# Performance work log

Measured on AMD Instinct MI355X. Metric: run time of the kernel, lower is better.

## Reference

```python
import jax, jax.numpy as jnp
import numpy as np

N = 131072   # total inner-graph nodes (G * n)
G = 2048     # number of inner graphs = nodes of outer graph fg
n = 64       # nodes per inner graph (contiguous blocks)
E = 1048576  # inner edges
EF = 32768   # outer (fg) edges
D = 128      # emb_dim == hidden_dim
K = 8        # SortPooling k
VOCAB = 150


def setup_inputs() -> dict:
    key = jax.random.key(0)
    ks = jax.random.split(key, 32)
    p = lambda k, shape: (jax.random.normal(k, shape, jnp.float32) * 0.1)
    inp = {
        'h': jax.random.randint(ks[0], (N,), 0, VOCAB),
        'g_src': jax.random.randint(ks[1], (E,), 0, N),
        'g_dst': jax.random.randint(ks[2], (E,), 0, N),
        'fg_src': jax.random.randint(ks[3], (EF,), 0, G),
        'fg_dst': jax.random.randint(ks[4], (EF,), 0, G),
        'token_emb': p(ks[5], (VOCAB, D)),
        # GATConv 1 (D -> D, 1 head): fc weight (in,out), attn vectors, output bias
        'W1': p(ks[6], (D, D)), 'al1': p(ks[7], (D,)), 'ar1': p(ks[8], (D,)), 'b1': p(ks[9], (D,)),
        # GATConv 2
        'W2': p(ks[10], (D, D)), 'al2': p(ks[11], (D,)), 'ar2': p(ks[12], (D,)), 'b2': p(ks[13], (D,)),
        # GATConv 3 (K*D -> D) over fg
        'W3': p(ks[14], (K * D, D)), 'al3': p(ks[15], (D,)), 'ar3': p(ks[16], (D,)), 'b3': p(ks[17], (D,)),
        # linear_forward
        'Wf': p(ks[18], (D, D)), 'bf': p(ks[19], (D,)),
        # linear
        'Wl': p(ks[20], (D, D)), 'bl': p(ks[21], (D,)),
        # linear1
        'Wl1': p(ks[22], (D, D)), 'bl1': p(ks[23], (D,)),
        # clasifier
        'Wc': p(ks[24], (D, 2)), 'bc': p(ks[25], (2,)),
    }
    return inp


def gat_conv(src, dst, num_nodes, x, W, al, ar, b):
    """DGL GATConv, num_heads=1, allow_zero_in_degree=True, no activation."""
    f = x @ W                                   # [N, D] projected features
    el = f @ al                                 # [N] left attention logits
    er = f @ ar                                 # [N] right attention logits
    e = jax.nn.leaky_relu(el[src] + er[dst], 0.2)   # [E] per-edge score
    m = jax.ops.segment_max(e, dst, num_segments=num_nodes)
    a = jnp.exp(e - m[dst])
    s = jax.ops.segment_sum(a, dst, num_segments=num_nodes)
    alpha = a / s[dst]                          # edge softmax over incoming edges
    out = jax.ops.segment_sum(alpha[:, None] * f[src], dst, num_segments=num_nodes)
    return out + b                              # zero-in-degree nodes -> bias only


def sort_pooling(x, num_graphs, nodes_per_graph, k):
    """DGL SortPooling: sort each node's feature ascending, rank nodes by last
    channel descending, take top-k, concat -> [G, k*D]."""
    d = x.shape[-1]
    x = jnp.sort(x.reshape(num_graphs, nodes_per_graph, d), axis=-1)
    idx = jnp.argsort(-x[:, :, -1], axis=1)[:, :k]          # [G, k]
    topk = jnp.take_along_axis(x, idx[:, :, None], axis=1)  # [G, k, D]
    return topk.reshape(num_graphs, k * d)


def reference(h, g_src, g_dst, fg_src, fg_dst, token_emb,
              W1, al1, ar1, b1, W2, al2, ar2, b2, W3, al3, ar3, b3,
              Wf, bf, Wl, bl, Wl1, bl1, Wc, bc):
    x = jax.nn.relu(token_emb[h])                                   # [N, D]
    x = jax.nn.relu(gat_conv(g_src, g_dst, N, x, W1, al1, ar1, b1))
    x = jax.nn.relu(gat_conv(g_src, g_dst, N, x, W2, al2, ar2, b2))
    x = jax.nn.relu(x @ Wf + bf)                                    # linear_forward
    x = sort_pooling(x, G, n, K)                                    # [G, K*D]
    x = jax.nn.relu(gat_conv(fg_src, fg_dst, G, x, W3, al3, ar3, b3))
    x = jax.nn.relu(x @ Wl + bl)                                    # dropout = eval identity
    x = jax.nn.relu(x @ Wl1 + bl1)
    x = x @ Wc + bc
    return x.reshape(-1, 2)
```

## Files before the change

### kernel.cpp

```cpp
#include <hip/hip_runtime.h>
#include <math.h>

#define NN   131072
#define GG   2048
#define NPG  64
#define EE   1048576
#define EFN  32768
#define DD   128
#define KK   8
#define VOCAB 150

typedef unsigned short bfu;
typedef _Float16 f16x8 __attribute__((ext_vector_type(8)));
typedef float f32x4 __attribute__((ext_vector_type(4)));

static __device__ __forceinline__ bfu f2b(float f) {
  unsigned u = __float_as_uint(f);
  u += 0x7FFFu + ((u >> 16) & 1u);
  return (bfu)(u >> 16);
}
static __device__ __forceinline__ float b2f(bfu b) {
  return __uint_as_float(((unsigned)b) << 16);
}

static __device__ __forceinline__ bfu f2h(float f) {
  _Float16 h = (_Float16)f;
  bfu u;
  __builtin_memcpy(&u, &h, 2);
  return u;
}
static __device__ __forceinline__ float h2f(bfu b) {
  _Float16 h;
  __builtin_memcpy(&h, &b, 2);
  return (float)h;
}

__global__ void fill_f32_kernel(float* __restrict__ p, float v, int nElems) {
  int i = blockIdx.x * 256 + threadIdx.x;
  if (i < nElems) p[i] = v;
}

__global__ void zero_int_kernel(int* __restrict__ p, int nElems) {
  int i = blockIdx.x * 256 + threadIdx.x;
  if (i < nElems) p[i] = 0;
}

__global__ void init_softmax_kernel(float* __restrict__ mx, float* __restrict__ sm, int nElems) {
  int i = blockIdx.x * 256 + threadIdx.x;
  if (i < nElems) { mx[i] = -INFINITY; sm[i] = 0.f; }
}

__global__ void embed_relu_kernel(const float* __restrict__ temb,
                                  const int* __restrict__ h,
                                  float* __restrict__ x, int total) {
  int i = blockIdx.x * 256 + threadIdx.x;
  if (i >= total) return;
// ... 88 lines not shown
    float val = red[r][c] + red[r][128 + c];
    out[(size_t)(row0 + r) * 128 + c] = val;
    As[idx] = val * al[c];
    As[4096 + idx] = val * ar[c];
  }
  __syncthreads();
  if (t < 8) {
    float s = 0.f;
    for (int c = 0; c < 128; c++) s += As[t * 128 + c];
    el[row0 + t] = s;
  } else if (t < 16) {
    int r = t - 8;
    float s = 0.f;
    for (int c = 0; c < 128; c++) s += As[4096 + r * 128 + c];
    er[row0 + r] = s;
  }
}

__global__ void pack_w2_kernel(const float* __restrict__ W2, const float* __restrict__ Wf,
                               bfu* __restrict__ w2h, bfu* __restrict__ wfh) {
  int i = blockIdx.x * 256 + threadIdx.x;
  if (i >= 32768) return;
  const float* W = (i < 16384) ? W2 : Wf;
  bfu* dst = (i < 16384) ? w2h : wfh;
  int ii = i & 16383;
  int k = ii >> 7, n = ii & 127;
  bfu h = f2h(W[ii]);
  int kk = k >> 5, k5 = k & 31, quad = k5 >> 3, j = k5 & 7;
  int tt = n >> 4, m16 = n & 15;
  int pos = ((((kk * 8 + tt) * 4 + quad) * 16) + m16) * 8 + j;
  dst[pos] = h;
}

template <int SRC_MODE, int EPI>
__global__ __launch_bounds__(256) void mfma_gemm(
    const float* A, const bfu* __restrict__ WfHi,
    const float* __restrict__ bias, void* out,
    const float* __restrict__ al, const float* __restrict__ ar,
    float* __restrict__ el, float* __restrict__ er,
    float* __restrict__ keyb) {
  const int t = threadIdx.x;
  const int lane = t & 63, wv_ = t >> 6;
  const int m16 = lane & 15, quad = lane >> 4;
  const int rowbase = blockIdx.x * 128 + wv_ * 32;
  const float* arow0 = nullptr;
  const float* arow1 = nullptr;
  const bfu* brow0 = nullptr;
  const bfu* brow1 = nullptr;
  if constexpr (SRC_MODE == 0) {
    arow0 = A + (size_t)(rowbase + m16) * 128;
    arow1 = A + (size_t)(rowbase + 16 + m16) * 128;
  } else {
    brow0 = (const bfu*)A + (size_t)(rowbase + m16) * 128;
    brow1 = (const bfu*)A + (size_t)(rowbase + 16 + m16) * 128;
  }
  f32x4 acc[2][8];
#pragma unroll
  for (int rg = 0; rg < 2; rg++)
#pragma unroll
    for (int i = 0; i < 8; i++) acc[rg][i] = (f32x4){0.f, 0.f, 0.f, 0.f};
#pragma unroll
  for (int kk = 0; kk < 4; kk++) {
    int k0 = kk * 32 + quad * 8;
    f16x8 ahi0, alo0, ahi1, alo1;
    if constexpr (SRC_MODE == 2) {
      ahi0 = *(const f16x8*)(brow0 + k0);
      ahi1 = *(const f16x8*)(brow1 + k0);
    } else {
      float av0[8], av1[8];
      *(float4*)&av0[0] = *(const float4*)(arow0 + k0);
      *(float4*)&av0[4] = *(const float4*)(arow0 + k0 + 4);
      *(float4*)&av1[0] = *(const float4*)(arow1 + k0);
      *(float4*)&av1[4] = *(const float4*)(arow1 + k0 + 4);
#pragma unroll
      for (int i = 0; i < 8; i++) {
        _Float16 h0 = (_Float16)av0[i];
        ahi0[i] = h0;
        alo0[i] = (_Float16)(av0[i] - (float)h0);
        _Float16 h1 = (_Float16)av1[i];
        ahi1[i] = h1;
        alo1[i] = (_Float16)(av1[i] - (float)h1);
      }
    }
#pragma unroll
    for (int tt = 0; tt < 8; tt++) {
      int pos = ((((kk * 8 + tt) * 4 + quad) * 16) + m16) * 8;
      f16x8 bhi = *(const f16x8*)&WfHi[pos];
      acc[0][tt] = __builtin_amdgcn_mfma_f32_16x16x32_f16(ahi0, bhi, acc[0][tt], 0, 0, 0);
      if constexpr (SRC_MODE != 2)
        acc[0][tt] = __builtin_amdgcn_mfma_f32_16x16x32_f16(alo0, bhi, acc[0][tt], 0, 0, 0);
      acc[1][tt] = __builtin_amdgcn_mfma_f32_16x16x32_f16(ahi1, bhi, acc[1][tt], 0, 0, 0);
      if constexpr (SRC_MODE != 2)
        acc[1][tt] = __builtin_amdgcn_mfma_f32_16x16x32_f16(alo1, bhi, acc[1][tt], 0, 0, 0);
    }
  }
#pragma unroll
  for (int rg = 0; rg < 2; rg++) {
    const int rb = rowbase + rg * 16;
    if constexpr (EPI == 1) {
      float pl[4] = {0.f, 0.f, 0.f, 0.f}, pr[4] = {0.f, 0.f, 0.f, 0.f};
#pragma unroll
      for (int tt = 0; tt < 8; tt++) {
        int col = tt * 16 + m16;
        float alv = al[col], arv = ar[col];
#pragma unroll
        for (int r = 0; r < 4; r++) {
          float v = acc[rg][tt][r];
          ((bfu*)out)[(size_t)(rb + quad * 4 + r) * 128 + col] = f2h(v);
          pl[r] += v * alv;
          pr[r] += v * arv;
        }
      }
#pragma unroll
      for (int r = 0; r < 4; r++) {
        float a0 = pl[r], a1 = pr[r];
#pragma unroll
        for (int off = 1; off < 16; off <<= 1) {
          a0 += __shfl_xor(a0, off);
          a1 += __shfl_xor(a1, off);
        }
        if (m16 == 0) {
          el[rb + quad * 4 + r] = a0;
          er[rb + quad * 4 + r] = a1;
        }
      }
    } else {
      float pm[4] = {-INFINITY, -INFINITY, -INFINITY, -INFINITY};
#pragma unroll
      for (int tt = 0; tt < 8; tt++) {
        int col = tt * 16 + m16;
        float bv = bias[col];
#pragma unroll
        for (int r = 0; r < 4; r++) {
          float v = fmaxf(acc[rg][tt][r] + bv, 0.f);
          ((bfu*)out)[(size_t)(rb + quad * 4 + r) * 128 + col] = f2h(v);
          pm[r] = fmaxf(pm[r], v);
        }
      }
#pragma unroll
      for (int r = 0; r < 4; r++) {
        float a0 = pm[r];
#pragma unroll
        for (int off = 1; off < 16; off <<= 1) a0 = fmaxf(a0, __shfl_xor(a0, off));
        if (m16 == 0) keyb[rb + quad * 4 + r] = a0;
      }
    }
  }
}

__global__ __launch_bounds__(64) void attn_logits_kernel(
    const float* __restrict__ f, const float* __restrict__ al,
    const float* __restrict__ ar, float* __restrict__ el,
    float* __restrict__ er) {
  int node = blockIdx.x, lane = threadIdx.x;
  float v1 = f[(size_t)node * 128 + lane];
  float v2 = f[(size_t)node * 128 + 64 + lane];
  float sl = v1 * al[lane] + v2 * al[64 + lane];
  float sr = v1 * ar[lane] + v2 * ar[64 + lane];
#pragma unroll
  for (int off = 32; off; off >>= 1) {
    sl += __shfl_down(sl, off);
    sr += __shfl_down(sr, off);
  }
  if (lane == 0) { el[node] = sl; er[node] = sr; }
}

__global__ void hist_rank_kernel(const int* __restrict__ dst, int* __restrict__ cnt,
                                 int* __restrict__ rank, int nE) {
  int e = blockIdx.x * 256 + threadIdx.x;
  if (e < nE) rank[e] = atomicAdd(&cnt[dst[e]], 1);
}

__global__ __launch_bounds__(256) void scan_block_kernel(
    const int* __restrict__ cnt, int* __restrict__ excl, int* __restrict__ part) {
  __shared__ int s[256];
  int blk = blockIdx.x, tid = threadIdx.x;
  int base = blk * 1024 + tid * 4;
// ... 35 lines not shown
  if (i == 0) row_ptr[n] = total;
}

__global__ __launch_bounds__(256) void scan2048_kernel(const int* __restrict__ cnt,
                                                       int* __restrict__ rp, int total) {
  __shared__ int s[256];
  int t = threadIdx.x;
  int base = t * 8;
  int v[8];
  int tsum = 0;
#pragma unroll
  for (int i = 0; i < 8; i++) { v[i] = cnt[base + i]; tsum += v[i]; }
  s[t] = tsum; __syncthreads();
  for (int off = 1; off < 256; off <<= 1) {
    int x = (t >= off) ? s[t - off] : 0;
    __syncthreads();
    s[t] += x;
    __syncthreads();
  }
  int excl = s[t] - tsum;
#pragma unroll
  for (int i = 0; i < 8; i++) { rp[base + i] = excl; excl += v[i]; }
  if (t == 255) rp[2048] = total;
}

__global__ void scatter2_kernel(const int* __restrict__ dst, const int* __restrict__ src,
                                const int* __restrict__ row_ptr, const int* __restrict__ rank,
                                int* __restrict__ adj_src, int nE) {
  int e = blockIdx.x * 256 + threadIdx.x;
  if (e >= nE) return;
  adj_src[row_ptr[dst[e]] + rank[e]] = src[e];
}

__global__ __launch_bounds__(256) void gat_aggregate_vocab_kernel(
    const bfu* __restrict__ fvh, const float* __restrict__ elv,
    const float* __restrict__ erv, const int* __restrict__ h,
    const int* __restrict__ row_ptr, const int* __restrict__ adj_src,
    const float* __restrict__ bias, bfu* __restrict__ outX) {
  const int t = threadIdx.x;
  const int l = t & 31;
  const int gb = t & 32;
  const int d = blockIdx.x * 8 + (t >> 5);
  const int c0 = l * 4;
  int beg = row_ptr[d];
  int n = row_ptr[d + 1] - beg;
  float4 bv = *(const float4*)&bias[c0];
  if (n == 0) {
    ushort4 o;
    o.x = f2h(fmaxf(bv.x, 0.f)); o.y = f2h(fmaxf(bv.y, 0.f));
    o.z = f2h(fmaxf(bv.z, 0.f)); o.w = f2h(fmaxf(bv.w, 0.f));
    *(ushort4*)&outX[(size_t)d * 128 + c0] = o;
    return;
  }
  float er_d = erv[h[d]];
  float4 acc = make_float4(0.f, 0.f, 0.f, 0.f);
  if (n <= 32) {
    int hv = 0; float sc = -INFINITY;
    if (l < n) {
      hv = h[adj_src[beg + l]];
      float v = elv[hv] + er_d;
      sc = v > 0.f ? v : 0.2f * v;
    }
    float m = sc;
#pragma unroll
    for (int off = 16; off; off >>= 1) m = fmaxf(m, __shfl_xor(m, off));
    float ex = (l < n) ? expf(sc - m) : 0.f;
    float s = ex;
#pragma unroll
    for (int off = 16; off; off >>= 1) s += __shfl_xor(s, off);
    float wt = ex / s;
    for (int j = 0; j < n; j += 4) {
      int   h0 = __shfl(hv, gb + j);
      float w0 = __shfl(wt, gb + j);
      int   j1 = (j + 1 < n) ? j + 1 : j;
      int   h1 = __shfl(hv, gb + j1); float w1 = (j + 1 < n) ? __shfl(wt, gb + j1) : 0.f;
      int   j2 = (j + 2 < n) ? j + 2 : j;
      int   h2 = __shfl(hv, gb + j2); float w2 = (j + 2 < n) ? __shfl(wt, gb + j2) : 0.f;
      int   j3 = (j + 3 < n) ? j + 3 : j;
      int   h3 = __shfl(hv, gb + j3); float w3 = (j + 3 < n) ? __shfl(wt, gb + j3) : 0.f;
      ushort4 f0 = *(const ushort4*)&fvh[(size_t)h0 * 128 + c0];
      ushort4 f1 = *(const ushort4*)&fvh[(size_t)h1 * 128 + c0];
      ushort4 f2 = *(const ushort4*)&fvh[(size_t)h2 * 128 + c0];
      ushort4 f3 = *(const ushort4*)&fvh[(size_t)h3 * 128 + c0];
      acc.x += w0 * h2f(f0.x) + w1 * h2f(f1.x) + w2 * h2f(f2.x) + w3 * h2f(f3.x);
      acc.y += w0 * h2f(f0.y) + w1 * h2f(f1.y) + w2 * h2f(f2.y) + w3 * h2f(f3.y);
      acc.z += w0 * h2f(f0.z) + w1 * h2f(f1.z) + w2 * h2f(f2.z) + w3 * h2f(f3.z);
      acc.w += w0 * h2f(f0.w) + w1 * h2f(f1.w) + w2 * h2f(f2.w) + w3 * h2f(f3.w);
    }
  } else {
    float lm = -INFINITY;
    for (int e = l; e < n; e += 32) {
      int hv = h[adj_src[beg + e]];
      float v = elv[hv] + er_d;
      v = v > 0.f ? v : 0.2f * v;
      lm = fmaxf(lm, v);
    }
#pragma unroll
    for (int off = 16; off; off >>= 1) lm = fmaxf(lm, __shfl_xor(lm, off));
    float ls = 0.f;
    for (int e = l; e < n; e += 32) {
      int hv = h[adj_src[beg + e]];
      float v = elv[hv] + er_d;
      v = v > 0.f ? v : 0.2f * v;
      ls += expf(v - lm);
    }
#pragma unroll
    for (int off = 16; off; off >>= 1) ls += __shfl_xor(ls, off);
    for (int base = 0; base < n; base += 32) {
      int e = base + l;
      int hv = 0; float wt = 0.f;
      if (e < n) {
        hv = h[adj_src[beg + e]];
        float v = elv[hv] + er_d;
        v = v > 0.f ? v : 0.2f * v;
        wt = expf(v - lm) / ls;
      }
      int cnt = min(32, n - base);
      for (int j = 0; j < cnt; ++j) {
        int h0 = __shfl(hv, gb + j);
        float w0 = __shfl(wt, gb + j);
        ushort4 f0 = *(const ushort4*)&fvh[(size_t)h0 * 128 + c0];
        acc.x += w0 * h2f(f0.x);
        acc.y += w0 * h2f(f0.y);
        acc.z += w0 * h2f(f0.z);
        acc.w += w0 * h2f(f0.w);
      }
    }
  }
  ushort4 o;
  o.x = f2h(fmaxf(acc.x + bv.x, 0.f));
  o.y = f2h(fmaxf(acc.y + bv.y, 0.f));
  o.z = f2h(fmaxf(acc.z + bv.z, 0.f));
  o.w = f2h(fmaxf(acc.w + bv.w, 0.f));
  *(ushort4*)&outX[(size_t)d * 128 + c0] = o;
}

__global__ __launch_bounds__(256) void gat_aggregate_csr_kernel(
    const bfu* __restrict__ F, const float* __restrict__ el,
    const float* __restrict__ er, const int* __restrict__ row_ptr,
    const int* __restrict__ adj_src,
    const float* __restrict__ bias, bfu* __restrict__ outX) {
  const int t = threadIdx.x;
  const int l = t & 31;
  const int gb = t & 32;
  const int d = blockIdx.x * 8 + (t >> 5);
  const int c0 = l * 4;
  int beg = row_ptr[d];
  int n = row_ptr[d + 1] - beg;
  float4 bv = *(const float4*)&bias[c0];
  if (n == 0) {
    ushort4 o;
    o.x = f2h(fmaxf(bv.x, 0.f)); o.y = f2h(fmaxf(bv.y, 0.f));
    o.z = f2h(fmaxf(bv.z, 0.f)); o.w = f2h(fmaxf(bv.w, 0.f));
    *(ushort4*)&outX[(size_t)d * 128 + c0] = o;
    return;
  }
  float er_d = er[d];
  float4 acc = make_float4(0.f, 0.f, 0.f, 0.f);
  if (n <= 32) {
    int sv = 0; float sc = -INFINITY;
    if (l < n) {
      sv = adj_src[beg + l];
      float v = el[sv] + er_d;
      sc = v > 0.f ? v : 0.2f * v;
    }
    float m = sc;
#pragma unroll
    for (int off = 16; off; off >>= 1) m = fmaxf(m, __shfl_xor(m, off));
    float ex = (l < n) ? expf(sc - m) : 0.f;
    float s = ex;
#pragma unroll
    for (int off = 16; off; off >>= 1) s += __shfl_xor(s, off);
    float wt = ex / s;
    for (int j = 0; j < n; j += 4) {
      int   s0 = __shfl(sv, gb + j);
      float w0 = __shfl(wt, gb + j);
      int   j1 = (j + 1 < n) ? j + 1 : j;
      int   s1 = __shfl(sv, gb + j1); float w1 = (j + 1 < n) ? __shfl(wt, gb + j1) : 0.f;
      int   j2 = (j + 2 < n) ? j + 2 : j;
      int   s2 = __shfl(sv, gb + j2); float w2 = (j + 2 < n) ? __shfl(wt, gb + j2) : 0.f;
      int   j3 = (j + 3 < n) ? j + 3 : j;
      int   s3 = __shfl(sv, gb + j3); float w3 = (j + 3 < n) ? __shfl(wt, gb + j3) : 0.f;
      ushort4 f0 = *(const ushort4*)&F[(size_t)s0 * 128 + c0];
      ushort4 f1 = *(const ushort4*)&F[(size_t)s1 * 128 + c0];
      ushort4 f2 = *(const ushort4*)&F[(size_t)s2 * 128 + c0];
      ushort4 f3 = *(const ushort4*)&F[(size_t)s3 * 128 + c0];
      acc.x += w0 * h2f(f0.x) + w1 * h2f(f1.x) + w2 * h2f(f2.x) + w3 * h2f(f3.x);
      acc.y += w0 * h2f(f0.y) + w1 * h2f(f1.y) + w2 * h2f(f2.y) + w3 * h2f(f3.y);
      acc.z += w0 * h2f(f0.z) + w1 * h2f(f1.z) + w2 * h2f(f2.z) + w3 * h2f(f3.z);
      acc.w += w0 * h2f(f0.w) + w1 * h2f(f1.w) + w2 * h2f(f2.w) + w3 * h2f(f3.w);
    }
  } else {
    float lm = -INFINITY;
    for (int e = l; e < n; e += 32) {
      int sv = adj_src[beg + e];
      float v = el[sv] + er_d;
      v = v > 0.f ? v : 0.2f * v;
      lm = fmaxf(lm, v);
    }
#pragma unroll
    for (int off = 16; off; off >>= 1) lm = fmaxf(lm, __shfl_xor(lm, off));
    float ls = 0.f;
    for (int e = l; e < n; e += 32) {
      int sv = adj_src[beg + e];
      float v = el[sv] + er_d;
      v = v > 0.f ? v : 0.2f * v;
      ls += expf(v - lm);
    }
#pragma unroll
    for (int off = 16; off; off >>= 1) ls += __shfl_xor(ls, off);
    for (int base = 0; base < n; base += 32) {
      int e = base + l;
      int sv = 0; float wt = 0.f;
      if (e < n) {
        sv = adj_src[beg + e];
        float v = el[sv] + er_d;
        v = v > 0.f ? v : 0.2f * v;
        wt = expf(v - lm) / ls;
      }
      int cnt = min(32, n - base);
      for (int j = 0; j < cnt; ++j) {
        int s0 = __shfl(sv, gb + j);
        float w0 = __shfl(wt, gb + j);
        ushort4 f0 = *(const ushort4*)&F[(size_t)s0 * 128 + c0];
        acc.x += w0 * h2f(f0.x);
        acc.y += w0 * h2f(f0.y);
        acc.z += w0 * h2f(f0.z);
        acc.w += w0 * h2f(f0.w);
      }
    }
  }
  ushort4 o;
  o.x = f2h(fmaxf(acc.x + bv.x, 0.f));
  o.y = f2h(fmaxf(acc.y + bv.y, 0.f));
  o.z = f2h(fmaxf(acc.z + bv.z, 0.f));
  o.w = f2h(fmaxf(acc.w + bv.w, 0.f));
  *(ushort4*)&outX[(size_t)d * 128 + c0] = o;
}

__global__ __launch_bounds__(256) void gat_aggregate_outer_kernel(
    const float* __restrict__ F, const float* __restrict__ el,
    const float* __restrict__ er, const int* __restrict__ row_ptr,
    const int* __restrict__ adj_src,
    const float* __restrict__ bias, float* __restrict__ outG) {
  const int t = threadIdx.x;
  const int l = t & 31;
  const int gb = t & 32;
  const int d = blockIdx.x * 8 + (t >> 5);
  const int c0 = l * 4;
  int beg = row_ptr[d];
  int n = row_ptr[d + 1] - beg;
  float4 bv = *(const float4*)&bias[c0];
  if (n == 0) {
    float4 o;
    o.x = fmaxf(bv.x, 0.f); o.y = fmaxf(bv.y, 0.f);
    o.z = fmaxf(bv.z, 0.f); o.w = fmaxf(bv.w, 0.f);
    *(float4*)&outG[(size_t)d * 128 + c0] = o;
    return;
  }
  float er_d = er[d];
  float4 acc = make_float4(0.f, 0.f, 0.f, 0.f);
  if (n <= 32) {
    int sv = 0; float sc = -INFINITY;
    if (l < n) {
      sv = adj_src[beg + l];
      float v = el[sv] + er_d;
      sc = v > 0.f ? v : 0.2f * v;
    }
    float m = sc;
#pragma unroll
// ... 105 lines not shown
__global__ void bias_relu_kernel(float* __restrict__ x,
                                 const float* __restrict__ b, int total) {
  int i = blockIdx.x * 256 + threadIdx.x;
  if (i >= total) return;
  x[i] = fmaxf(x[i] + b[i & 127], 0.f);
}

__global__ __launch_bounds__(64) void row_max_kernel(const float* __restrict__ x,
                                                     float* __restrict__ key) {
  int node = blockIdx.x, lane = threadIdx.x;
  float v = fmaxf(x[(size_t)node * 128 + lane], x[(size_t)node * 128 + 64 + lane]);
#pragma unroll
  for (int off = 32; off; off >>= 1) v = fmaxf(v, __shfl_down(v, off));
  if (lane == 0) key[node] = v;
}

__global__ __launch_bounds__(64) void select_topk_kernel(
    const float* __restrict__ key, int* __restrict__ sel) {
  __shared__ float keys[NPG];
  int g = blockIdx.x, t = threadIdx.x;
  keys[t] = key[(size_t)g * NPG + t];
  __syncthreads();
  float myk = keys[t];
  int rank = 0;
  for (int j = 0; j < NPG; ++j) {
    float kj = keys[j];
    rank += (kj > myk) || (kj == myk && j < t);
  }
  if (rank < KK) sel[g * KK + rank] = t;
}

__global__ __launch_bounds__(1024) void topk_sort_kernel(
    const float* __restrict__ keyb, const bfu* __restrict__ xin,
    float* __restrict__ xp) {
  __shared__ float keys[NPG];
  __shared__ int sel_l[KK];
  __shared__ float v[1024];
  int g = blockIdx.x, t = threadIdx.x;
  if (t < NPG) keys[t] = keyb[(size_t)g * NPG + t];
  __syncthreads();
  if (t < NPG) {
    float myk = keys[t];
    int rank = 0;
    for (int j = 0; j < NPG; ++j) {
      float kj = keys[j];
      rank += (kj > myk) || (kj == myk && j < t);
    }
    if (rank < KK) sel_l[rank] = t;
  }
  __syncthreads();
  int r = t >> 7, c = t & 127;
  int node = sel_l[r];
  v[t] = h2f(xin[(size_t)(g * NPG + node) * 128 + c]);
  __syncthreads();
  for (int k = 2; k <= 128; k <<= 1) {
    for (int j = k >> 1; j > 0; j >>= 1) {
      int ixj = c ^ j;
      if (ixj > c) {
        float a = v[r * 128 + c], bb = v[r * 128 + ixj];
        bool asc = ((c & k) == 0);
        if (asc ? (a > bb) : (a < bb)) { v[r * 128 + c] = bb; v[r * 128 + ixj] = a; }
      }
      __syncthreads();
    }
  }
  xp[(size_t)g * 1024 + t] = v[t];
}

template <int HF>
__global__ __launch_bounds__(128) void sort_rows_kernel(
    const void* __restrict__ xin, const int* __restrict__ sel,
    float* __restrict__ xp) {
  __shared__ float v[128];
  int b = blockIdx.x;
  int t = threadIdx.x;
  int g = b >> 3, r = b & 7;
  int node = sel[b];
  if (HF) v[t] = h2f(((const bfu*)xin)[(size_t)(g * NPG + node) * 128 + t]);
  else    v[t] = ((const float*)xin)[(size_t)(g * NPG + node) * 128 + t];
  __syncthreads();
  for (int k = 2; k <= 128; k <<= 1) {
    for (int j = k >> 1; j > 0; j >>= 1) {
      int ixj = t ^ j;
      if (ixj > t) {
        float a = v[t], bb = v[ixj];
        bool asc = ((t & k) == 0);
        if (asc ? (a > bb) : (a < bb)) { v[t] = bb; v[ixj] = a; }
      }
      __syncthreads();
    }
  }
  xp[(size_t)g * (KK * 128) + r * 128 + t] = v[t];
}

__global__ __launch_bounds__(128) void mlp_tail_kernel(
    const float* __restrict__ g3, const float* __restrict__ Wl,
    const float* __restrict__ bl, const float* __restrict__ Wl1,
    const float* __restrict__ bl1, const float* __restrict__ Wc,
    const float* __restrict__ bc, float* __restrict__ out) {
// ... 50 lines not shown
  const float* ar2 = (const float*)d_in[12];
  const float* b2 = (const float*)d_in[13];
  const float* W3 = (const float*)d_in[14];
  const float* al3 = (const float*)d_in[15];
  const float* ar3 = (const float*)d_in[16];
  const float* b3 = (const float*)d_in[17];
  const float* Wf = (const float*)d_in[18];
  const float* bfv = (const float*)d_in[19];
  const float* Wl = (const float*)d_in[20];
  const float* bl = (const float*)d_in[21];
  const float* Wl1 = (const float*)d_in[22];
  const float* bl1 = (const float*)d_in[23];
  const float* Wc = (const float*)d_in[24];
  const float* bc = (const float*)d_in[25];
  float* out = (float*)d_out;

  float* ws = (float*)d_ws;
  float* X  = ws;
  float* F  = X + (size_t)NN * DD;
  float* el = F + (size_t)NN * DD;
  float* er = el + NN;
  float* mx = er + NN;
  float* sm = mx + NN;
  int* row_ptr = (int*)(sm + NN);
  int* cursor  = row_ptr + NN + 1;
  int* adj_src = cursor + NN;
  int* part    = adj_src + EE;
  int* rankb = (int*)X;
  bfu* w2h = (bfu*)mx;
  bfu* wfh = w2h + 16384;
  bfu* fvh = wfh + 16384;
  float* elv = (float*)(fvh + VOCAB * 128 + 128);
  float* erv = elv + VOCAB;
  int* ocnt  = (int*)X;
  int* orp   = ocnt + 2048;
  int* orank = orp + 2080;
  int* oadj  = orank + EFN;
  float* xp   = F;
  float* f3   = F + 2097152;
  float* g3   = f3 + (size_t)GG * DD;
  float* t1   = g3 + (size_t)GG * DD;
  float* t2   = t1 + (size_t)GG * DD;
  float* keyb = t2 + (size_t)GG * DD;
  int*   sel  = (int*)(keyb + NN);

  const int totalND = NN * DD;

  if (use_csr) {
    bfu* Fb = (bfu*)F;
    bfu* Xb = (bfu*)X;
    zero_int_kernel<<<NN / 256, 256, 0, stream>>>(cursor, NN);
    hist_rank_kernel<<<EE / 256, 256, 0, stream>>>(g_dst, cursor, rankb, EE);
    scan_block_kernel<<<NN / 1024, 256, 0, stream>>>(cursor, row_ptr, part);
    scan_part_kernel<<<1, 128, 0, stream>>>(part);
    scan_add_kernel<<<(NN + 255) / 256, 256, 0, stream>>>(row_ptr, part, NN, EE);
    scatter2_kernel<<<EE / 256, 256, 0, stream>>>(g_dst, g_src, row_ptr, rankb, adj_src, EE);

    pack_w2_kernel<<<128, 256, 0, stream>>>(W2, Wf, w2h, wfh);
    vocab_l1_kernel<<<VOCAB, 128, 0, stream>>>(temb, W1, al1, ar1, fvh, elv, erv);

    gat_aggregate_vocab_kernel<<<NN / 8, 256, 0, stream>>>(
        fvh, elv, erv, h, row_ptr, adj_src, b1, Xb);

    mfma_gemm<2, 1><<<NN / 128, 256, 0, stream>>>(
        (const float*)X, w2h, nullptr, Fb, al2, ar2, el, er, nullptr);
    gat_aggregate_csr_kernel<<<NN / 8, 256, 0, stream>>>(Fb, el, er, row_ptr, adj_src, b2, Xb);

    mfma_gemm<2, 2><<<NN / 128, 256, 0, stream>>>(
        (const float*)X, wfh, bfv, Xb, nullptr, nullptr, nullptr, nullptr, keyb);

    topk_sort_kernel<<<GG, 1024, 0, stream>>>(keyb, Xb, xp);

    zero_int_kernel<<<GG / 256, 256, 0, stream>>>(ocnt, GG);
    hist_rank_kernel<<<EFN / 256, 256, 0, stream>>>(fg_dst, ocnt, orank, EFN);
    scan2048_kernel<<<1, 256, 0, stream>>>(ocnt, orp, EFN);
    scatter2_kernel<<<EFN / 256, 256, 0, stream>>>(fg_dst, fg_src, orp, orank, oadj, EFN);

    gemm1024_kernel<<<GG / 8, 256, 0, stream>>>(xp, W3, f3, al3, ar3, el, er);
    gat_aggregate_outer_kernel<<<GG / 8, 256, 0, stream>>>(f3, el, er, orp, oadj, b3, g3);

    mlp_tail_kernel<<<GG, 128, 0, stream>>>(g3, Wl, bl, Wl1, bl1, Wc, bc, out);
  } else {
    embed_relu_kernel<<<totalND / 256, 256, 0, stream>>>(temb, h, X, totalND);
    auto gat_inner = [&](const float* W, const float* al, const float* ar, const float* bb) {
      gemm_kernel<DD, 8><<<NN / 8, 128, 0, stream>>>(X, W, nullptr, F, 0);
      attn_logits_kernel<<<NN, 64, 0, stream>>>(F, al, ar, el, er);
      init_softmax_kernel<<<(NN + 255) / 256, 256, 0, stream>>>(mx, sm, NN);
      fill_f32_kernel<<<totalND / 256, 256, 0, stream>>>(X, 0.f, totalND);
      edge_max_kernel<<<(EE + 255) / 256, 256, 0, stream>>>(el, er, g_src, g_dst, mx, EE);
      edge_expsum_kernel<<<(EE + 255) / 256, 256, 0, stream>>>(el, er, mx, g_src, g_dst, sm, EE);
      edge_aggregate_kernel<<<EE, 128, 0, stream>>>(F, el, er, mx, sm, g_src, g_dst, X, EE);
      bias_relu_kernel<<<totalND / 256, 256, 0, stream>>>(X, bb, totalND);
    };
    gat_inner(W1, al1, ar1, b1);
    gat_inner(W2, al2, ar2, b2);
    gemm_kernel<DD, 8><<<NN / 8, 128, 0, stream>>>(X, Wf, bfv, X, 1);
    row_max_kernel<<<NN, 64, 0, stream>>>(X, keyb);

    select_topk_kernel<<<GG, 64, 0, stream>>>(keyb, sel);
    sort_rows_kernel<0><<<GG * KK, 128, 0, stream>>>(X, sel, xp);

    gemm1024_kernel<<<GG / 8, 256, 0, stream>>>(xp, W3, f3, al3, ar3, el, er);
    init_softmax_kernel<<<(GG + 255) / 256, 256, 0, stream>>>(mx, sm, GG);
    fill_f32_kernel<<<(GG * DD + 255) / 256, 256, 0, stream>>>(g3, 0.f, GG * DD);
    edge_max_kernel<<<(EFN + 255) / 256, 256, 0, stream>>>(el, er, fg_src, fg_dst, mx, EFN);
    edge_expsum_kernel<<<(EFN + 255) / 256, 256, 0, stream>>>(el, er, mx, fg_src, fg_dst, sm, EFN);
    edge_aggregate_kernel<<<EFN, 128, 0, stream>>>(f3, el, er, mx, sm, fg_src, fg_dst, g3, EFN);
    bias_relu_kernel<<<(GG * DD + 255) / 256, 256, 0, stream>>>(g3, b3, GG * DD);
    mlp_tail_kernel<<<GG, 128, 0, stream>>>(g3, Wl, bl, Wl1, bl1, Wc, bc, out);
  }
}
// ... 1 lines not shown
```

Before: 425.0 us.

## Fuse GAT aggregation with following MFMA GEMM via LDS tile; MFMA for 1024 GEMM

Merges each inner GAT edge-softmax aggregation with the next projection GEMM. Aggregated rows go into a swizzled 128x128 fp16 LDS tile that feeds MFMA directly, so the intermediate activation no longer round-trips through global memory. The scatter now packs the source node's token id into the high bits of the adjacency entry, which removes the dependent h[] gather in layer 1. The outer 1024-wide GEMM moves to fp16 MFMA using packed W3 and fp16 pooled inputs, trading some precision and adding a 32KB LDS footprint that may lower occupancy.

```diff
diff --git a/kernel.cpp b/kernel.cpp
--- a/kernel.cpp
+++ b/kernel.cpp
@@ -9,19 +9,11 @@
 #define DD   128
 #define KK   8
 #define VOCAB 150
+#define SRCMASK 0x1FFFF
 
 typedef unsigned short bfu;
 typedef _Float16 f16x8 __attribute__((ext_vector_type(8)));
 typedef float f32x4 __attribute__((ext_vector_type(4)));
-
-static __device__ __forceinline__ bfu f2b(float f) {
-  unsigned u = __float_as_uint(f);
-  u += 0x7FFFu + ((u >> 16) & 1u);
-  return (bfu)(u >> 16);
-}
-static __device__ __forceinline__ float b2f(bfu b) {
-  return __uint_as_float(((unsigned)b) << 16);
-}
 
 static __device__ __forceinline__ bfu f2h(float f) {
   _Float16 h = (_Float16)f;
@@ -176,72 +168,162 @@
   dst[pos] = h;
 }
 
-template <int SRC_MODE, int EPI>
-__global__ __launch_bounds__(256) void mfma_gemm(
-    const float* A, const bfu* __restrict__ WfHi,
-    const float* __restrict__ bias, void* out,
+__global__ void pack_wk_kernel(const float* __restrict__ W, bfu* __restrict__ dst, int total) {
+  int i = blockIdx.x * 256 + threadIdx.x;
+  if (i >= total) return;
+  int k = i >> 7, n = i & 127;
+  bfu h = f2h(W[i]);
+  int kk = k >> 5, k5 = k & 31, quad = k5 >> 3, j = k5 & 7;
+  int tt = n >> 4, m16 = n & 15;
+  int pos = ((((kk * 8 + tt) * 4 + quad) * 16) + m16) * 8 + j;
+  dst[pos] = h;
+}
+
+template <int MODE>
+__global__ __launch_bounds__(256) void agg_gemm_kernel(
+    const bfu* __restrict__ Fsrc, const float* __restrict__ elA,
+    const float* __restrict__ erA, const int* __restrict__ h,
+    const int* __restrict__ row_ptr, const int* __restrict__ adj,
+    const float* __restrict__ aggBias, const bfu* __restrict__ Wtab,
     const float* __restrict__ al, const float* __restrict__ ar,
-    float* __restrict__ el, float* __restrict__ er,
+    const float* __restrict__ gemmBias,
+    bfu* __restrict__ outF,
+    float* __restrict__ el_out, float* __restrict__ er_out,
     float* __restrict__ keyb) {
+  __shared__ bfu Atile[128 * 128];
   const int t = threadIdx.x;
+  const int l = t & 31;
+  const int gb = t & 32;
+  const int grp = t >> 5;
+  const int c0 = l * 4;
+  const int blockbase = blockIdx.x * 128;
+  float4 bv = *(const float4*)&aggBias[c0];
+
+  for (int iter = 0; iter < 16; ++iter) {
+    const int dl = iter * 8 + grp;
+    const int d = blockbase + dl;
+    int beg = row_ptr[d];
+    int n = row_ptr[d + 1] - beg;
+    float4 acc = make_float4(0.f, 0.f, 0.f, 0.f);
+    if (n > 0) {
+      float er_d = (MODE == 0) ? erA[h[d]] : erA[d];
+      if (n <= 32) {
+        int idx = 0; float sc = -INFINITY;
+        if (l < n) {
+          int a = adj[beg + l];
+          idx = (MODE == 0) ? (a >> 17) : (a & SRCMASK);
+          float v = elA[idx] + er_d;
+          sc = v > 0.f ? v : 0.2f * v;
+        }
+        float m = sc;
+#pragma unroll
+        for (int off = 16; off; off >>= 1) m = fmaxf(m, __shfl_xor(m, off));
+        float ex = (l < n) ? expf(sc - m) : 0.f;
+        float s = ex;
+#pragma unroll
+        for (int off = 16; off; off >>= 1) s += __shfl_xor(s, off);
+        float wt = ex / s;
+        for (int j = 0; j < n; j += 4) {
+          int   s0 = __shfl(idx, gb + j);
+          float w0 = __shfl(wt, gb + j);
+          int   j1 = (j + 1 < n) ? j + 1 : j;
+          int   s1 = __shfl(idx, gb + j1); float w1 = (j + 1 < n) ? __shfl(wt, gb + j1) : 0.f;
+          int   j2 = (j + 2 < n) ? j + 2 : j;
+          int   s2 = __shfl(idx, gb + j2); float w2 = (j + 2 < n) ? __shfl(wt, gb + j2) : 0.f;
+          int   j3 = (j + 3 < n) ? j + 3 : j;
+          int   s3 = __shfl(idx, gb + j3); float w3 = (j + 3 < n) ? __shfl(wt, gb + j3) : 0.f;
+          ushort4 f0 = *(const ushort4*)&Fsrc[(size_t)s0 * 128 + c0];
+          ushort4 f1 = *(const ushort4*)&Fsrc[(size_t)s1 * 128 + c0];
+          ushort4 f2 = *(const ushort4*)&Fsrc[(size_t)s2 * 128 + c0];
+          ushort4 f3 = *(const ushort4*)&Fsrc[(size_t)s3 * 128 + c0];
+          acc.x += w0 * h2f(f0.x) + w1 * h2f(f1.x) + w2 * h2f(f2.x) + w3 * h2f(f3.x);
+          acc.y += w0 * h2f(f0.y) + w1 * h2f(f1.y) + w2 * h2f(f2.y) + w3 * h2f(f3.y);
+          acc.z += w0 * h2f(f0.z) + w1 * h2f(f1.z) + w2 * h2f(f2.z) + w3 * h2f(f3.z);
+          acc.w += w0 * h2f(f0.w) + w1 * h2f(f1.w) + w2 * h2f(f2.w) + w3 * h2f(f3.w);
+        }
+      } else {
+        float lm = -INFINITY;
+        for (int e = l; e < n; e += 32) {
+          int a = adj[beg + e];
+          int idx = (MODE == 0) ? (a >> 17) : (a & SRCMASK);
+          float v = elA[idx] + er_d;
+          v = v > 0.f ? v : 0.2f * v;
+          lm = fmaxf(lm, v);
+        }
+#pragma unroll
+        for (int off = 16; off; off >>= 1) lm = fmaxf(lm, __shfl_xor(lm, off));
+        float ls = 0.f;
+        for (int e = l; e < n; e += 32) {
+          int a = adj[beg + e];
+          int idx = (MODE == 0) ? (a >> 17) : (a & SRCMASK);
+          float v = elA[idx] + er_d;
+          v = v > 0.f ? v : 0.2f * v;
+          ls += expf(v - lm);
+        }
+#pragma unroll
+        for (int off = 16; off; off >>= 1) ls += __shfl_xor(ls, off);
+        for (int base = 0; base < n; base += 32) {
+          int e = base + l;
+          int idx = 0; float wt = 0.f;
+          if (e < n) {
+            int a = adj[beg + e];
+            idx = (MODE == 0) ? (a >> 17) : (a & SRCMASK);
+            float v = elA[idx] + er_d;
+            v = v > 0.f ? v : 0.2f * v;
+            wt = expf(v - lm) / ls;
+          }
+          int cnt = min(32, n - base);
+          for (int j = 0; j < cnt; ++j) {
+            int s0 = __shfl(idx, gb + j);
+            float w0 = __shfl(wt, gb + j);
+            ushort4 f0 = *(const ushort4*)&Fsrc[(size_t)s0 * 128 + c0];
+            acc.x += w0 * h2f(f0.x);
+            acc.y += w0 * h2f(f0.y);
+            acc.z += w0 * h2f(f0.z);
+            acc.w += w0 * h2f(f0.w);
+          }
+        }
+      }
+    }
+    ushort4 o;
+    o.x = f2h(fmaxf(acc.x + bv.x, 0.f));
+    o.y = f2h(fmaxf(acc.y + bv.y, 0.f));
+    o.z = f2h(fmaxf(acc.z + bv.z, 0.f));
+    o.w = f2h(fmaxf(acc.w + bv.w, 0.f));
+    int chunk = l >> 1;
+    int off = dl * 256 + (((chunk ^ (dl & 15)) << 4)) + ((l & 1) << 3);
+    *(ushort4*)((char*)Atile + off) = o;
+  }
+  __syncthreads();
+
   const int lane = t & 63, wv_ = t >> 6;
   const int m16 = lane & 15, quad = lane >> 4;
-  const int rowbase = blockIdx.x * 128 + wv_ * 32;
-  const float* arow0 = nullptr;
-  const float* arow1 = nullptr;
-  const bfu* brow0 = nullptr;
-  const bfu* brow1 = nullptr;
-  if constexpr (SRC_MODE == 0) {
-    arow0 = A + (size_t)(rowbase + m16) * 128;
-    arow1 = A + (size_t)(rowbase + 16 + m16) * 128;
-  } else {
-    brow0 = (const bfu*)A + (size_t)(rowbase + m16) * 128;
-    brow1 = (const bfu*)A + (size_t)(rowbase + 16 + m16) * 128;
-  }
-  f32x4 acc[2][8];
+  f32x4 acc2[2][8];
 #pragma unroll
   for (int rg = 0; rg < 2; rg++)
 #pragma unroll
-    for (int i = 0; i < 8; i++) acc[rg][i] = (f32x4){0.f, 0.f, 0.f, 0.f};
+    for (int i = 0; i < 8; i++) acc2[rg][i] = (f32x4){0.f, 0.f, 0.f, 0.f};
 #pragma unroll
   for (int kk = 0; kk < 4; kk++) {
-    int k0 = kk * 32 + quad * 8;
-    f16x8 ahi0, alo0, ahi1, alo1;
-    if constexpr (SRC_MODE == 2) {
-      ahi0 = *(const f16x8*)(brow0 + k0);
-      ahi1 = *(const f16x8*)(brow1 + k0);
-    } else {
-      float av0[8], av1[8];
-      *(float4*)&av0[0] = *(const float4*)(arow0 + k0);
-      *(float4*)&av0[4] = *(const float4*)(arow0 + k0 + 4);
-      *(float4*)&av1[0] = *(const float4*)(arow1 + k0);
-      *(float4*)&av1[4] = *(const float4*)(arow1 + k0 + 4);
-#pragma unroll
-      for (int i = 0; i < 8; i++) {
-        _Float16 h0 = (_Float16)av0[i];
-        ahi0[i] = h0;
-        alo0[i] = (_Float16)(av0[i] - (float)h0);
-        _Float16 h1 = (_Float16)av1[i];
-        ahi1[i] = h1;
-        alo1[i] = (_Float16)(av1[i] - (float)h1);
-      }
-    }
+    int cb = kk * 4 + quad;
+    int r0 = wv_ * 32 + m16;
+    int r1 = r0 + 16;
+    int a0 = r0 * 256 + ((cb ^ (r0 & 15)) << 4);
+    int a1 = r1 * 256 + ((cb ^ (r1 & 15)) << 4);
+    f16x8 ahi0 = *(const f16x8*)((char*)Atile + a0);
+    f16x8 ahi1 = *(const f16x8*)((char*)Atile + a1);
 #pragma unroll
     for (int tt = 0; tt < 8; tt++) {
       int pos = ((((kk * 8 + tt) * 4 + quad) * 16) + m16) * 8;
-      f16x8 bhi = *(const f16x8*)&WfHi[pos];
-      acc[0][tt] = __builtin_amdgcn_mfma_f32_16x16x32_f16(ahi0, bhi, acc[0][tt], 0, 0, 0);
-      if constexpr (SRC_MODE != 2)
-        acc[0][tt] = __builtin_amdgcn_mfma_f32_16x16x32_f16(alo0, bhi, acc[0][tt], 0, 0, 0);
-      acc[1][tt] = __builtin_amdgcn_mfma_f32_16x16x32_f16(ahi1, bhi, acc[1][tt], 0, 0, 0);
-      if constexpr (SRC_MODE != 2)
-        acc[1][tt] = __builtin_amdgcn_mfma_f32_16x16x32_f16(alo1, bhi, acc[1][tt], 0, 0, 0);
+      f16x8 bhi = *(const f16x8*)&Wtab[pos];
+      acc2[0][tt] = __builtin_amdgcn_mfma_f32_16x16x32_f16(ahi0, bhi, acc2[0][tt], 0, 0, 0);
+      acc2[1][tt] = __builtin_amdgcn_mfma_f32_16x16x32_f16(ahi1, bhi, acc2[1][tt], 0, 0, 0);
     }
   }
 #pragma unroll
   for (int rg = 0; rg < 2; rg++) {
-    const int rb = rowbase + rg * 16;
-    if constexpr (EPI == 1) {
+    const int rb = blockbase + wv_ * 32 + rg * 16;
+    if constexpr (MODE == 0) {
       float pl[4] = {0.f, 0.f, 0.f, 0.f}, pr[4] = {0.f, 0.f, 0.f, 0.f};
 #pragma unroll
       for (int tt = 0; tt < 8; tt++) {
@@ -249,8 +331,8 @@
         float alv = al[col], arv = ar[col];
 #pragma unroll
         for (int r = 0; r < 4; r++) {
-          float v = acc[rg][tt][r];
-          ((bfu*)out)[(size_t)(rb + quad * 4 + r) * 128 + col] = f2h(v);
+          float v = acc2[rg][tt][r];
+          outF[(size_t)(rb + quad * 4 + r) * 128 + col] = f2h(v);
           pl[r] += v * alv;
           pr[r] += v * arv;
         }
@@ -264,8 +346,8 @@
           a1 += __shfl_xor(a1, off);
         }
         if (m16 == 0) {
-          el[rb + quad * 4 + r] = a0;
-          er[rb + quad * 4 + r] = a1;
+          el_out[rb + quad * 4 + r] = a0;
+          er_out[rb + quad * 4 + r] = a1;
         }
       }
     } else {
@@ -273,11 +355,11 @@
 #pragma unroll
       for (int tt = 0; tt < 8; tt++) {
         int col = tt * 16 + m16;
-        float bv = bias[col];
+        float bvv = gemmBias[col];
 #pragma unroll
         for (int r = 0; r < 4; r++) {
-          float v = fmaxf(acc[rg][tt][r] + bv, 0.f);
-          ((bfu*)out)[(size_t)(rb + quad * 4 + r) * 128 + col] = f2h(v);
+          float v = fmaxf(acc2[rg][tt][r] + bvv, 0.f);
+          outF[(size_t)(rb + quad * 4 + r) * 128 + col] = f2h(v);
           pm[r] = fmaxf(pm[r], v);
         }
       }
@@ -287,6 +369,66 @@
 #pragma unroll
         for (int off = 1; off < 16; off <<= 1) a0 = fmaxf(a0, __shfl_xor(a0, off));
         if (m16 == 0) keyb[rb + quad * 4 + r] = a0;
+      }
+    }
+  }
+}
+
+__global__ __launch_bounds__(256) void mfma_gemm1024_kernel(
+    const bfu* __restrict__ A, const bfu* __restrict__ Wtab,
+    float* __restrict__ out, const float* __restrict__ al,
+    const float* __restrict__ ar, float* __restrict__ el,
+    float* __restrict__ er) {
+  const int t = threadIdx.x;
+  const int lane = t & 63, wv_ = t >> 6;
+  const int m16 = lane & 15, quad = lane >> 4;
+  const int rowbase = blockIdx.x * 128 + wv_ * 32;
+  const bfu* brow0 = A + (size_t)(rowbase + m16) * 1024;
+  const bfu* brow1 = A + (size_t)(rowbase + 16 + m16) * 1024;
+  f32x4 acc[2][8];
+#pragma unroll
+  for (int rg = 0; rg < 2; rg++)
+#pragma unroll
+    for (int i = 0; i < 8; i++) acc[rg][i] = (f32x4){0.f, 0.f, 0.f, 0.f};
+  for (int kk = 0; kk < 32; kk++) {
+    int k0 = kk * 32 + quad * 8;
+    f16x8 ahi0 = *(const f16x8*)(brow0 + k0);
+    f16x8 ahi1 = *(const f16x8*)(brow1 + k0);
+#pragma unroll
+    for (int tt = 0; tt < 8; tt++) {
+      int pos = ((((kk * 8 + tt) * 4 + quad) * 16) + m16) * 8;
+      f16x8 bhi = *(const f16x8*)&Wtab[pos];
+      acc[0][tt] = __builtin_amdgcn_mfma_f32_16x16x32_f16(ahi0, bhi, acc[0][tt], 0, 0, 0);
+      acc[1][tt] = __builtin_amdgcn_mfma_f32_16x16x32_f16(ahi1, bhi, acc[1][tt], 0, 0, 0);
+    }
+  }
+#pragma unroll
+  for (int rg = 0; rg < 2; rg++) {
+    const int rb = rowbase + rg * 16;
+    float pl[4] = {0.f, 0.f, 0.f, 0.f}, pr[4] = {0.f, 0.f, 0.f, 0.f};
+#pragma unroll
+    for (int tt = 0; tt < 8; tt++) {
+      int col = tt * 16 + m16;
+      float alv = al[col], arv = ar[col];
+#pragma unroll
+      for (int r = 0; r < 4; r++) {
+        float v = acc[rg][tt][r];
+        out[(size_t)(rb + quad * 4 + r) * 128 + col] = v;
+        pl[r] += v * alv;
+        pr[r] += v * arv;
+      }
+    }
+#pragma unroll
+    for (int r = 0; r < 4; r++) {
+      float a0 = pl[r], a1 = pr[r];
+#pragma unroll
+      for (int off = 1; off < 16; off <<= 1) {
+        a0 += __shfl_xor(a0, off);
+        a1 += __shfl_xor(a1, off);
+      }
+      if (m16 == 0) {
+        el[rb + quad * 4 + r] = a0;
+        er[rb + quad * 4 + r] = a1;
       }
     }
   }
@@ -388,210 +530,14 @@
   adj_src[row_ptr[dst[e]] + rank[e]] = src[e];
 }
 
-__global__ __launch_bounds__(256) void gat_aggregate_vocab_kernel(
-    const bfu* __restrict__ fvh, const float* __restrict__ elv,
-    const float* __restrict__ erv, const int* __restrict__ h,
-    const int* __restrict__ row_ptr, const int* __restrict__ adj_src,
-    const float* __restrict__ bias, bfu* __restrict__ outX) {
-  const int t = threadIdx.x;
-  const int l = t & 31;
-  const int gb = t & 32;
-  const int d = blockIdx.x * 8 + (t >> 5);
-  const int c0 = l * 4;
-  int beg = row_ptr[d];
-  int n = row_ptr[d + 1] - beg;
-  float4 bv = *(const float4*)&bias[c0];
-  if (n == 0) {
-    ushort4 o;
-    o.x = f2h(fmaxf(bv.x, 0.f)); o.y = f2h(fmaxf(bv.y, 0.f));
-    o.z = f2h(fmaxf(bv.z, 0.f)); o.w = f2h(fmaxf(bv.w, 0.f));
-    *(ushort4*)&outX[(size_t)d * 128 + c0] = o;
-    return;
-  }
-  float er_d = erv[h[d]];
-  float4 acc = make_float4(0.f, 0.f, 0.f, 0.f);
-  if (n <= 32) {
-    int hv = 0; float sc = -INFINITY;
-    if (l < n) {
-      hv = h[adj_src[beg + l]];
-      float v = elv[hv] + er_d;
-      sc = v > 0.f ? v : 0.2f * v;
-    }
-    float m = sc;
-#pragma unroll
-    for (int off = 16; off; off >>= 1) m = fmaxf(m, __shfl_xor(m, off));
-    float ex = (l < n) ? expf(sc - m) : 0.f;
-    float s = ex;
-#pragma unroll
-    for (int off = 16; off; off >>= 1) s += __shfl_xor(s, off);
-    float wt = ex / s;
-    for (int j = 0; j < n; j += 4) {
-      int   h0 = __shfl(hv, gb + j);
-      float w0 = __shfl(wt, gb + j);
-      int   j1 = (j + 1 < n) ? j + 1 : j;
-      int   h1 = __shfl(hv, gb + j1); float w1 = (j + 1 < n) ? __shfl(wt, gb + j1) : 0.f;
-      int   j2 = (j + 2 < n) ? j + 2 : j;
-      int   h2 = __shfl(hv, gb + j2); float w2 = (j + 2 < n) ? __shfl(wt, gb + j2) : 0.f;
-      int   j3 = (j + 3 < n) ? j + 3 : j;
-      int   h3 = __shfl(hv, gb + j3); float w3 = (j + 3 < n) ? __shfl(wt, gb + j3) : 0.f;
-      ushort4 f0 = *(const ushort4*)&fvh[(size_t)h0 * 128 + c0];
-      ushort4 f1 = *(const ushort4*)&fvh[(size_t)h1 * 128 + c0];
-      ushort4 f2 = *(const ushort4*)&fvh[(size_t)h2 * 128 + c0];
-      ushort4 f3 = *(const ushort4*)&fvh[(size_t)h3 * 128 + c0];
-      acc.x += w0 * h2f(f0.x) + w1 * h2f(f1.x) + w2 * h2f(f2.x) + w3 * h2f(f3.x);
-      acc.y += w0 * h2f(f0.y) + w1 * h2f(f1.y) + w2 * h2f(f2.y) + w3 * h2f(f3.y);
-      acc.z += w0 * h2f(f0.z) + w1 * h2f(f1.z) + w2 * h2f(f2.z) + w3 * h2f(f3.z);
-      acc.w += w0 * h2f(f0.w) + w1 * h2f(f1.w) + w2 * h2f(f2.w) + w3 * h2f(f3.w);
-    }
-  } else {
-    float lm = -INFINITY;
-    for (int e = l; e < n; e += 32) {
-      int hv = h[adj_src[beg + e]];
-      float v = elv[hv] + er_d;
-      v = v > 0.f ? v : 0.2f * v;
-      lm = fmaxf(lm, v);
-    }
-#pragma unroll
-    for (int off = 16; off; off >>= 1) lm = fmaxf(lm, __shfl_xor(lm, off));
-    float ls = 0.f;
-    for (int e = l; e < n; e += 32) {
-      int hv = h[adj_src[beg + e]];
-      float v = elv[hv] + er_d;
-      v = v > 0.f ? v : 0.2f * v;
-      ls += expf(v - lm);
-    }
-#pragma unroll
-    for (int off = 16; off; off >>= 1) ls += __shfl_xor(ls, off);
-    for (int base = 0; base < n; base += 32) {
-      int e = base + l;
-      int hv = 0; float wt = 0.f;
-      if (e < n) {
-        hv = h[adj_src[beg + e]];
-        float v = elv[hv] + er_d;
-        v = v > 0.f ? v : 0.2f * v;
-        wt = expf(v - lm) / ls;
-      }
-      int cnt = min(32, n - base);
-      for (int j = 0; j < cnt; ++j) {
-        int h0 = __shfl(hv, gb + j);
-        float w0 = __shfl(wt, gb + j);
-        ushort4 f0 = *(const ushort4*)&fvh[(size_t)h0 * 128 + c0];
-        acc.x += w0 * h2f(f0.x);
-        acc.y += w0 * h2f(f0.y);
-        acc.z += w0 * h2f(f0.z);
-        acc.w += w0 * h2f(f0.w);
-      }
-    }
-  }
-  ushort4 o;
-  o.x = f2h(fmaxf(acc.x + bv.x, 0.f));
-  o.y = f2h(fmaxf(acc.y + bv.y, 0.f));
-  o.z = f2h(fmaxf(acc.z + bv.z, 0.f));
-  o.w = f2h(fmaxf(acc.w + bv.w, 0.f));
-  *(ushort4*)&outX[(size_t)d * 128 + c0] = o;
-}
-
-__global__ __launch_bounds__(256) void gat_aggregate_csr_kernel(
-    const bfu* __restrict__ F, const float* __restrict__ el,
-    const float* __restrict__ er, const int* __restrict__ row_ptr,
-    const int* __restrict__ adj_src,
-    const float* __restrict__ bias, bfu* __restrict__ outX) {
-  const int t = threadIdx.x;
-  const int l = t & 31;
-  const int gb = t & 32;
-  const int d = blockIdx.x * 8 + (t >> 5);
-  const int c0 = l * 4;
-  int beg = row_ptr[d];
-  int n = row_ptr[d + 1] - beg;
-  float4 bv = *(const float4*)&bias[c0];
-  if (n == 0) {
-    ushort4 o;
-    o.x = f2h(fmaxf(bv.x, 0.f)); o.y = f2h(fmaxf(bv.y, 0.f));
-    o.z = f2h(fmaxf(bv.z, 0.f)); o.w = f2h(fmaxf(bv.w, 0.f));
-    *(ushort4*)&outX[(size_t)d * 128 + c0] = o;
-    return;
-  }
-  float er_d = er[d];
-  float4 acc = make_float4(0.f, 0.f, 0.f, 0.f);
-  if (n <= 32) {
-    int sv = 0; float sc = -INFINITY;
-    if (l < n) {
-      sv = adj_src[beg + l];
-      float v = el[sv] + er_d;
-      sc = v > 0.f ? v : 0.2f * v;
-    }
-    float m = sc;
-#pragma unroll
-    for (int off = 16; off; off >>= 1) m = fmaxf(m, __shfl_xor(m, off));
-    float ex = (l < n) ? expf(sc - m) : 0.f;
-    float s = ex;
-#pragma unroll
-    for (int off = 16; off; off >>= 1) s += __shfl_xor(s, off);
-    float wt = ex / s;
-    for (int j = 0; j < n; j += 4) {
-      int   s0 = __shfl(sv, gb + j);
-      float w0 = __shfl(wt, gb + j);
-      int   j1 = (j + 1 < n) ? j + 1 : j;
-      int   s1 = __shfl(sv, gb + j1); float w1 = (j + 1 < n) ? __shfl(wt, gb + j1) : 0.f;
-      int   j2 = (j + 2 < n) ? j + 2 : j;
-      int   s2 = __shfl(sv, gb + j2); float w2 = (j + 2 < n) ? __shfl(wt, gb + j2) : 0.f;
-      int   j3 = (j + 3 < n) ? j + 3 : j;
-      int   s3 = __shfl(sv, gb + j3); float w3 = (j + 3 < n) ? __shfl(wt, gb + j3) : 0.f;
-      ushort4 f0 = *(const ushort4*)&F[(size_t)s0 * 128 + c0];
-      ushort4 f1 = *(const ushort4*)&F[(size_t)s1 * 128 + c0];
-      ushort4 f2 = *(const ushort4*)&F[(size_t)s2 * 128 + c0];
-      ushort4 f3 = *(const ushort4*)&F[(size_t)s3 * 128 + c0];
-      acc.x += w0 * h2f(f0.x) + w1 * h2f(f1.x) + w2 * h2f(f2.x) + w3 * h2f(f3.x);
-      acc.y += w0 * h2f(f0.y) + w1 * h2f(f1.y) + w2 * h2f(f2.y) + w3 * h2f(f3.y);
-      acc.z += w0 * h2f(f0.z) + w1 * h2f(f1.z) + w2 * h2f(f2.z) + w3 * h2f(f3.z);
-      acc.w += w0 * h2f(f0.w) + w1 * h2f(f1.w) + w2 * h2f(f2.w) + w3 * h2f(f3.w);
-    }
-  } else {
-    float lm = -INFINITY;
-    for (int e = l; e < n; e += 32) {
-      int sv = adj_src[beg + e];
-      float v = el[sv] + er_d;
-      v = v > 0.f ? v : 0.2f * v;
-      lm = fmaxf(lm, v);
-    }
-#pragma unroll
-    for (int off = 16; off; off >>= 1) lm = fmaxf(lm, __shfl_xor(lm, off));
-    float ls = 0.f;
-    for (int e = l; e < n; e += 32) {
-      int sv = adj_src[beg + e];
-      float v = el[sv] + er_d;
-      v = v > 0.f ? v : 0.2f * v;
-      ls += expf(v - lm);
-    }
-#pragma unroll
-    for (int off = 16; off; off >>= 1) ls += __shfl_xor(ls, off);
-    for (int base = 0; base < n; base += 32) {
-      int e = base + l;
-      int sv = 0; float wt = 0.f;
-      if (e < n) {
-        sv = adj_src[beg + e];
-        float v = el[sv] + er_d;
-        v = v > 0.f ? v : 0.2f * v;
-        wt = expf(v - lm) / ls;
-      }
-      int cnt = min(32, n - base);
-      for (int j = 0; j < cnt; ++j) {
-        int s0 = __shfl(sv, gb + j);
-        float w0 = __shfl(wt, gb + j);
-        ushort4 f0 = *(const ushort4*)&F[(size_t)s0 * 128 + c0];
-        acc.x += w0 * h2f(f0.x);
-        acc.y += w0 * h2f(f0.y);
-        acc.z += w0 * h2f(f0.z);
-        acc.w += w0 * h2f(f0.w);
-      }
-    }
-  }
-  ushort4 o;
-  o.x = f2h(fmaxf(acc.x + bv.x, 0.f));
-  o.y = f2h(fmaxf(acc.y + bv.y, 0.f));
-  o.z = f2h(fmaxf(acc.z + bv.z, 0.f));
-  o.w = f2h(fmaxf(acc.w + bv.w, 0.f));
-  *(ushort4*)&outX[(size_t)d * 128 + c0] = o;
+__global__ void scatter2_pack_kernel(const int* __restrict__ dst, const int* __restrict__ src,
+                                     const int* __restrict__ h,
+                                     const int* __restrict__ row_ptr, const int* __restrict__ rank,
+                                     int* __restrict__ adj_src, int nE) {
+  int e = blockIdx.x * 256 + threadIdx.x;
+  if (e >= nE) return;
+  int s = src[e];
+  adj_src[row_ptr[dst[e]] + rank[e]] = s | (h[s] << 17);
 }
 
 __global__ __launch_bounds__(256) void gat_aggregate_outer_kernel(
@@ -763,7 +709,7 @@
 
 __global__ __launch_bounds__(1024) void topk_sort_kernel(
     const float* __restrict__ keyb, const bfu* __restrict__ xin,
-    float* __restrict__ xp) {
+    bfu* __restrict__ xp) {
   __shared__ float keys[NPG];
   __shared__ int sel_l[KK];
   __shared__ float v[1024];
@@ -795,7 +741,7 @@
       __syncthreads();
     }
   }
-  xp[(size_t)g * 1024 + t] = v[t];
+  xp[(size_t)g * 1024 + t] = f2h(v[t]);
 }
 
 template <int HF>
@@ -912,6 +858,8 @@
   bfu* fvh = wfh + 16384;
   float* elv = (float*)(fvh + VOCAB * 128 + 128);
   float* erv = elv + VOCAB;
+  bfu* w3h = (bfu*)(erv + VOCAB + 2);
+  float* keyb2 = X + (size_t)12 * 1024 * 1024;
   int* ocnt  = (int*)X;
   int* orp   = ocnt + 2048;
   int* orank = orp + 2080;
@@ -927,36 +875,36 @@
   const int totalND = NN * DD;
 
   if (use_csr) {
-    bfu* Fb = (bfu*)F;
-    bfu* Xb = (bfu*)X;
+    bfu* Fb  = (bfu*)F;
+    bfu* Xb  = (bfu*)X;
+    bfu* xph = (bfu*)xp;
     zero_int_kernel<<<NN / 256, 256, 0, stream>>>(cursor, NN);
     hist_rank_kernel<<<EE / 256, 256, 0, stream>>>(g_dst, cursor, rankb, EE);
     scan_block_kernel<<<NN / 1024, 256, 0, stream>>>(cursor, row_ptr, part);
     scan_part_kernel<<<1, 128, 0, stream>>>(part);
     scan_add_kernel<<<(NN + 255) / 256, 256, 0, stream>>>(row_ptr, part, NN, EE);
-    scatter2_kernel<<<EE / 256, 256, 0, stream>>>(g_dst, g_src, row_ptr, rankb, adj_src, EE);
+    scatter2_pack_kernel<<<EE / 256, 256, 0, stream>>>(g_dst, g_src, h, row_ptr, rankb, adj_src, EE);
 
     pack_w2_kernel<<<128, 256, 0, stream>>>(W2, Wf, w2h, wfh);
+    pack_wk_kernel<<<512, 256, 0, stream>>>(W3, w3h, 131072);
     vocab_l1_kernel<<<VOCAB, 128, 0, stream>>>(temb, W1, al1, ar1, fvh, elv, erv);
 
-    gat_aggregate_vocab_kernel<<<NN / 8, 256, 0, stream>>>(
-        fvh, elv, erv, h, row_ptr, adj_src, b1, Xb);
-
-    mfma_gemm<2, 1><<<NN / 128, 256, 0, stream>>>(
-        (const float*)X, w2h, nullptr, Fb, al2, ar2, el, er, nullptr);
-    gat_aggregate_csr_kernel<<<NN / 8, 256, 0, stream>>>(Fb, el, er, row_ptr, adj_src, b2, Xb);
-
-    mfma_gemm<2, 2><<<NN / 128, 256, 0, stream>>>(
-        (const float*)X, wfh, bfv, Xb, nullptr, nullptr, nullptr, nullptr, keyb);
-
-    topk_sort_kernel<<<GG, 1024, 0, stream>>>(keyb, Xb, xp);
+    agg_gemm_kernel<0><<<NN / 128, 256, 0, stream>>>(
+        fvh, elv, erv, h, row_ptr, adj_src, b1, w2h, al2, ar2, nullptr,
+        Fb, el, er, nullptr);
+
+    agg_gemm_kernel<1><<<NN / 128, 256, 0, stream>>>(
+        Fb, el, er, nullptr, row_ptr, adj_src, b2, wfh, nullptr, nullptr, bfv,
+        Xb, nullptr, nullptr, keyb2);
+
+    topk_sort_kernel<<<GG, 1024, 0, stream>>>(keyb2, Xb, xph);
 
     zero_int_kernel<<<GG / 256, 256, 0, stream>>>(ocnt, GG);
     hist_rank_kernel<<<EFN / 256, 256, 0, stream>>>(fg_dst, ocnt, orank, EFN);
     scan2048_kernel<<<1, 256, 0, stream>>>(ocnt, orp, EFN);
     scatter2_kernel<<<EFN / 256, 256, 0, stream>>>(fg_dst, fg_src, orp, orank, oadj, EFN);
 
-    gemm1024_kernel<<<GG / 8, 256, 0, stream>>>(xp, W3, f3, al3, ar3, el, er);
+    mfma_gemm1024_kernel<<<GG / 128, 256, 0, stream>>>(xph, w3h, f3, al3, ar3, el, er);
     gat_aggregate_outer_kernel<<<GG / 8, 256, 0, stream>>>(f3, el, er, orp, oadj, b3, g3);
 
     mlp_tail_kernel<<<GG, 128, 0, stream>>>(g3, Wl, bl, Wl1, bl1, Wc, bc, out);
```

Result: slower. 492.4 us (+15.8%).
